# Optimization experiments

Hardware: AMD Instinct MI355X
Metric: run time of the kernel (lower is better)

The kernel has to match this reference:

```python
import jax, jax.numpy as jnp
import numpy as np

B, L, H, E = 8, 1024, 8, 64
HIST = 512


def setup_inputs() -> dict:
    key = jax.random.key(0)
    ks = jax.random.split(key, 6)
    shp = (B, L, H, E)
    q, k, v, qd, kd, vd = (jax.random.normal(kk, shp, dtype=jnp.float32) for kk in ks)
    # DoubleTriangularCausalMask surrogate: strictly-upper-triangular causal mask (diagonal=1)
    attn_mask = jnp.triu(jnp.ones((L, L), dtype=bool), k=1)[None, None]  # (1,1,L,S)
    return {
        "queries": q, "keys": k, "values": v,
        "queries_drawn": qd, "keys_drawn": kd, "values_drawn": vd,
        "attn_mask": attn_mask, "history_len": HIST,
    }


def reference(queries, keys, values, queries_drawn, keys_drawn, values_drawn, attn_mask, history_len):
    # drawn_y=True branch of FullFixedTimeCausalConstructiveAttention with history_len set.
    B, L, H, E = queries.shape
    scale = 1.0 / float(np.sqrt(E))
    hist = history_len
    idx = jnp.arange(hist, L)

    # queries[:, hist:] = queries_drawn[:, hist:]
    q_eff = jnp.concatenate([queries[:, :hist], queries_drawn[:, hist:]], axis=1)

    scores = jnp.einsum('blhe,bshe->bhls', q_eff, keys)  # (B,H,L,S)
    # diagonal positions l>=hist use drawn keys: q_eff[l] . keys_drawn[l]
    diag_scores = jnp.einsum('blhe,blhe->bhl', q_eff[:, hist:], keys_drawn[:, hist:])
    scores = scores.at[:, :, idx, idx].set(diag_scores)

    scores = jnp.where(attn_mask, -jnp.inf, scores)
    A = jax.nn.softmax(scale * scores, axis=-1)  # (B,H,L,S); dropout rate 0 in eval

    # values substitution on the diagonal (l==s, l>=hist) is a rank-1 correction;
    # avoids materializing the torch (B,H,D,L,S) repeated tensor.
    V = jnp.einsum('bhls,bshd->blhd', A, values)
    diag_A = A[:, :, idx, idx]                      # (B,H,L-hist)
    delta = values_drawn[:, hist:] - values[:, hist:]  # (B,L-hist,H,D)
    V = V.at[:, hist:].add(jnp.transpose(diag_A, (0, 2, 1))[..., None] * delta)
    return V
```

## Files before the change

kernel.cpp:

```cpp
#include <hip/hip_runtime.h>

#define LL   1024
#define HH   8
#define EE   64
#define KSTR 72

#define SCALE2 0.18033688011112043f

typedef _Float16 f16;
typedef _Float16 v8h  __attribute__((ext_vector_type(8)));
typedef _Float16 h2   __attribute__((ext_vector_type(2)));
typedef float    v4f  __attribute__((ext_vector_type(4)));
typedef int      v2i  __attribute__((ext_vector_type(2)));

union U8 { v8h v; h2 h[4]; };

__device__ __forceinline__ float fexp2(float x) {
#if __has_builtin(__builtin_amdgcn_exp2f)
  return __builtin_amdgcn_exp2f(x);
#else
  return __expf(x * 0.6931471805599453f);
#endif
}

__device__ __forceinline__ h2 pkh2(float a, float b) {
#if __has_builtin(__builtin_amdgcn_cvt_pkrtz)
  return __builtin_bit_cast(h2, __builtin_amdgcn_cvt_pkrtz(a, b));
#else
  h2 r; r[0] = (f16)a; r[1] = (f16)b; return r;
#endif
}

__device__ __forceinline__ float red4max(float x) {
#if __has_builtin(__builtin_amdgcn_permlane16_swap) && __has_builtin(__builtin_amdgcn_permlane32_swap)
  int xi = __float_as_int(x);
  v2i a = __builtin_amdgcn_permlane16_swap(xi, xi, false, false);
  float m = fmaxf(__int_as_float(a.x), __int_as_float(a.y));
  int mi = __float_as_int(m);
  v2i b = __builtin_amdgcn_permlane32_swap(mi, mi, false, false);
  return fmaxf(__int_as_float(b.x), __int_as_float(b.y));
#else
  x = fmaxf(x, __shfl_xor(x, 16));
  return fmaxf(x, __shfl_xor(x, 32));
#endif
}

__device__ __forceinline__ float red4sum(float x) {
#if __has_builtin(__builtin_amdgcn_permlane16_swap) && __has_builtin(__builtin_amdgcn_permlane32_swap)
  int xi = __float_as_int(x);
  v2i a = __builtin_amdgcn_permlane16_swap(xi, xi, false, false);
  float s = __int_as_float(a.x) + __int_as_float(a.y);
  int si = __float_as_int(s);
  v2i b = __builtin_amdgcn_permlane32_swap(si, si, false, false);
  return __int_as_float(b.x) + __int_as_float(b.y);
#else
  x += __shfl_xor(x, 16);
  return x + __shfl_xor(x, 32);
#endif
}

__device__ __forceinline__ void load16f(const float* __restrict__ p, float* __restrict__ f) {
  const float4* p4 = reinterpret_cast<const float4*>(p);
  float4 a = p4[0], b = p4[1], c = p4[2], d = p4[3];
  f[0]=a.x;  f[1]=a.y;  f[2]=a.z;  f[3]=a.w;
  f[4]=b.x;  f[5]=b.y;  f[6]=b.z;  f[7]=b.w;
  f[8]=c.x;  f[9]=c.y;  f[10]=c.z; f[11]=c.w;
  f[12]=d.x; f[13]=d.y; f[14]=d.z; f[15]=d.w;
}

__device__ __forceinline__ void load8f(const float* __restrict__ p, float* __restrict__ f) {
  const float4* p4 = reinterpret_cast<const float4*>(p);
  float4 a = p4[0], b = p4[1];
  f[0]=a.x; f[1]=a.y; f[2]=a.z; f[3]=a.w;
  f[4]=b.x; f[5]=b.y; f[6]=b.z; f[7]=b.w;
}

struct TileState {
  v4f   o[4];
  float m, l, pd;
};

__device__ __forceinline__ void softmax_pack(
    TileState& st, const v4f* __restrict__ S, bool dt, bool drawn, float zdq,
    int qlocal, const int* __restrict__ kb, int lq, U8& A0, U8& A1)
{
  float z[4][4];
#pragma unroll
  for (int nb = 0; nb < 4; ++nb)
#pragma unroll
    for (int r = 0; r < 4; ++r) z[nb][r] = S[nb][r] * SCALE2;

  if (dt) {
#pragma unroll
    for (int nb = 0; nb < 4; ++nb) {
#pragma unroll
      for (int r = 0; r < 4; ++r) {
        const int kl = kb[nb] + r;
        if (kl > qlocal)                 z[nb][r] = -1e30f;
        else if (drawn && kl == qlocal)  z[nb][r] = zdq;
      }
    }
  }

  float a0 = fmaxf(fmaxf(z[0][0], z[0][1]), fmaxf(z[0][2], z[0][3]));
  float a1 = fmaxf(fmaxf(z[1][0], z[1][1]), fmaxf(z[1][2], z[1][3]));
  float a2 = fmaxf(fmaxf(z[2][0], z[2][1]), fmaxf(z[2][2], z[2][3]));
  float a3 = fmaxf(fmaxf(z[3][0], z[3][1]), fmaxf(z[3][2], z[3][3]));
  const float mx = red4max(fmaxf(fmaxf(a0, a1), fmaxf(a2, a3)));

  const float mn = fmaxf(st.m, mx);
  const float al = fexp2(st.m - mn);
  st.m = mn;

  float p[4][4], rsum = 0.f, pdl = 0.f;
#pragma unroll
  for (int nb = 0; nb < 4; ++nb) {
#pragma unroll
    for (int r = 0; r < 4; ++r) {
      const float pv = fexp2(z[nb][r] - mn);
      p[nb][r] = pv;
      rsum += pv;
      if (dt && drawn && (kb[nb] + r) == qlocal) pdl = pv;
    }
  }
  rsum = red4sum(rsum);
  if (dt && drawn) st.pd = red4sum(pdl);
  st.l = st.l * al + rsum;
#pragma unroll
  for (int nb = 0; nb < 4; ++nb)
#pragma unroll
    for (int r = 0; r < 4; ++r) st.o[nb][r] *= al;

  h2 wq[4][2];
#pragma unroll
  for (int nb = 0; nb < 4; ++nb) {
    wq[nb][0] = pkh2(p[nb][0], p[nb][1]);
    wq[nb][1] = pkh2(p[nb][2], p[nb][3]);
  }
  const bool swp = (lq & 1);
  A0.h[0] = swp ? wq[1][0] : wq[0][0];
  A0.h[1] = swp ? wq[1][1] : wq[0][1];
  A0.h[2] = swp ? wq[0][0] : wq[1][0];
  A0.h[3] = swp ? wq[0][1] : wq[1][1];
  A1.h[0] = swp ? wq[3][0] : wq[2][0];
  A1.h[1] = swp ? wq[3][1] : wq[2][1];
  A1.h[2] = swp ? wq[2][0] : wq[3][0];
  A1.h[3] = swp ? wq[2][1] : wq[3][1];
}

extern "C" __global__ __launch_bounds__(256, 2)
void ftcca_pair2(const float* __restrict__ Q,  const float* __restrict__ K,
                 const float* __restrict__ V,  const float* __restrict__ Qd,
                 const float* __restrict__ Kd, const float* __restrict__ Vd,
                 float* __restrict__ out)
{
  __shared__ f16   Ks[64 * KSTR];
  __shared__ f16   Vt[64 * KSTR];
  __shared__ float zdiag[64];

  const int bh  = blockIdx.x & 63;
  const int a   = blockIdx.x >> 6;
  const int qtA = 15 - a;
  const int qtB = a;
  const int b   = bh >> 3, h = bh & 7;
  const int t   = threadIdx.x;
  const int w    = t >> 6;
  const int lane = t & 63;
  const int ln   = lane & 15;
  const int lq   = lane >> 4;
  const int rs   = t >> 2;
  const int es0  = (t & 3) * 16;
  const int vr0  = (t >> 3) * 2;
  const int vd0  = (t & 7) * 8;

  const size_t base = ((size_t)b * LL * HH + h) * EE;
  const int ROWF = HH * EE;

  const int q2 = ln >> 2;
  int rk[4], kb[4];
  rk[0] = ln + ((q2 + 1) >> 1) * 8;
  rk[1] = ln + 4 + (q2 >> 1) * 8;
  rk[2] = rk[0] + 32;
  rk[3] = rk[1] + 32;
  kb[0] = 4 * lq + ((lq + 1) >> 1) * 8;
  kb[1] = 4 * lq + 4 + (lq >> 1) * 8;
  kb[2] = kb[0] + 32;
  kb[3] = kb[1] + 32;

  {
    const int l = qtA * 64 + rs;
    const float* qrow = Qd + base + (size_t)l * ROWF + es0;
    const float* krow = Kd + base + (size_t)l * ROWF + es0;
    float par = 0.f;
#pragma unroll
    for (int i = 0; i < 16; ++i) par += qrow[i] * krow[i];
    par += __shfl_xor(par, 1);
    par += __shfl_xor(par, 2);
    if ((t & 3) == 0) zdiag[rs] = SCALE2 * par;
  }

  const int rowt_q = w * 16 + ln;
  v8h qfA[2], qfB[2];
  {
    const float* pa = Qd + base + (size_t)(qtA * 64 + rowt_q) * ROWF;
    const float* pb = Q  + base + (size_t)(qtB * 64 + rowt_q) * ROWF;
#pragma unroll
    for (int c = 0; c < 2; ++c) {
      const float* xa = pa + 32 * c + 8 * lq;
      const float* xb = pb + 32 * c + 8 * lq;
#pragma unroll
      for (int j = 0; j < 8; ++j) { qfA[c][j] = (f16)xa[j]; qfB[c][j] = (f16)xb[j]; }
    }
  }

  TileState stA, stB;
#pragma unroll
  for (int nb = 0; nb < 4; ++nb) { stA.o[nb] = (v4f){0,0,0,0}; stB.o[nb] = (v4f){0,0,0,0}; }
  stA.m = -1e30f; stA.l = 0.f; stA.pd = 0.f;
  stB.m = -1e30f; stB.l = 0.f; stB.pd = 0.f;

  const int qlocal = w * 16 + ln;

  float tk[16], tv[16];
  load16f(K + base + (size_t)rs * ROWF + es0, tk);
  load8f(V + base + (size_t)vr0 * ROWF + vd0, tv);
  load8f(V + base + (size_t)(vr0 + 1) * ROWF + vd0, tv + 8);

  for (int i = 0; i <= qtA; ++i) {
    __syncthreads();
    {
      v8h k0, k1;
#pragma unroll
      for (int j = 0; j < 8; ++j) { k0[j] = (f16)tk[j]; k1[j] = (f16)tk[8 + j]; }
      v8h* kd0 = reinterpret_cast<v8h*>(&Ks[rs * KSTR + es0]);
      kd0[0] = k0;
      kd0[1] = k1;
      const int vswz = vr0 >> 3;
#pragma unroll
      for (int dd = 0; dd < 8; ++dd) {
        const int d  = vd0 + dd;
        const int ch = (vswz ^ (d >> 3)) & 7;
        h2 val; val[0] = (f16)tv[dd]; val[1] = (f16)tv[8 + dd];
        *reinterpret_cast<h2*>(&Vt[d * KSTR + ch * 8 + (vr0 & 7)]) = val;
      }
    }
    __syncthreads();

    if (i < qtA) {
      const size_t r0 = (size_t)((i + 1) * 64);
      load16f(K + base + (r0 + rs) * ROWF + es0, tk);
      load8f(V + base + (r0 + vr0) * ROWF + vd0, tv);
      load8f(V + base + (r0 + vr0 + 1) * ROWF + vd0, tv + 8);
    }

    const bool doB = (i <= qtB);
    const bool dtA = (i == qtA);
    const bool dtB = (i == qtB);

    v8h k0f[4], k1f[4];
#pragma unroll
    for (int nb = 0; nb < 4; ++nb) {
      const f16* krow = &Ks[rk[nb] * KSTR + 8 * lq];
      k0f[nb] = *reinterpret_cast<const v8h*>(krow);
      k1f[nb] = *reinterpret_cast<const v8h*>(krow + 32);
    }

    v4f SA[4], SB[4];
#pragma unroll
    for (int nb = 0; nb < 4; ++nb) {
      v4f acc = (v4f){0.f, 0.f, 0.f, 0.f};
      acc = __builtin_amdgcn_mfma_f32_16x16x32_f16(k0f[nb], qfA[0], acc, 0, 0, 0);
      acc = __builtin_amdgcn_mfma_f32_16x16x32_f16(k1f[nb], qfA[1], acc, 0, 0, 0);
      SA[nb] = acc;
    }
    if (doB) {
#pragma unroll
      for (int nb = 0; nb < 4; ++nb) {
        v4f acc = (v4f){0.f, 0.f, 0.f, 0.f};
        acc = __builtin_amdgcn_mfma_f32_16x16x32_f16(k0f[nb], qfB[0], acc, 0, 0, 0);
        acc = __builtin_amdgcn_mfma_f32_16x16x32_f16(k1f[nb], qfB[1], acc, 0, 0, 0);
        SB[nb] = acc;
      }
    }

    U8 pA0, pA1, pB0, pB1;
    const float zdq = dtA ? zdiag[qlocal] : 0.f;
    softmax_pack(stA, SA, dtA, true,  zdq, qlocal, kb, lq, pA0, pA1);
    if (doB)
      softmax_pack(stB, SB, dtB, false, 0.f, qlocal, kb, lq, pB0, pB1);

#pragma unroll
    for (int nb = 0; nb < 4; ++nb) {
      const int d   = nb * 16 + ln;
      const int dsw = (d >> 3) & 7;
      const f16* vbase = &Vt[d * KSTR];
      v8h v0 = *reinterpret_cast<const v8h*>(vbase + (((lq    ) ^ dsw) & 7) * 8);
      v8h v1 = *reinterpret_cast<const v8h*>(vbase + (((lq + 4) ^ dsw) & 7) * 8);
      stA.o[nb] = __builtin_amdgcn_mfma_f32_16x16x32_f16(v0, pA0.v, stA.o[nb], 0, 0, 0);
      stA.o[nb] = __builtin_amdgcn_mfma_f32_16x16x32_f16(v1, pA1.v, stA.o[nb], 0, 0, 0);
      if (doB) {
        stB.o[nb] = __builtin_amdgcn_mfma_f32_16x16x32_f16(v0, pB0.v, stB.o[nb], 0, 0, 0);
        stB.o[nb] = __builtin_amdgcn_mfma_f32_16x16x32_f16(v1, pB1.v, stB.o[nb], 0, 0, 0);
      }
    }
  }

  {
    const float inv = 1.f / stA.l;
    const float pdinv = stA.pd * inv;
    const int lrow = qtA * 64 + w * 16 + ln;
#pragma unroll
    for (int nb = 0; nb < 4; ++nb) {
      const int d0 = nb * 16 + lq * 4;
      const size_t g = base + (size_t)lrow * ROWF + d0;
      float4 vd4 = *reinterpret_cast<const float4*>(Vd + g);
      float4 v4  = *reinterpret_cast<const float4*>(V + g);
      float4 o4;
      o4.x = stA.o[nb][0] * inv + pdinv * (vd4.x - v4.x);
      o4.y = stA.o[nb][1] * inv + pdinv * (vd4.y - v4.y);
      o4.z = stA.o[nb][2] * inv + pdinv * (vd4.z - v4.z);
      o4.w = stA.o[nb][3] * inv + pdinv * (vd4.w - v4.w);
      *reinterpret_cast<float4*>(out + g) = o4;
    }
  }
  {
    const float inv = 1.f / stB.l;
    const int lrow = qtB * 64 + w * 16 + ln;
#pragma unroll
    for (int nb = 0; nb < 4; ++nb) {
      const int d0 = nb * 16 + lq * 4;
      const size_t g = base + (size_t)lrow * ROWF + d0;
      float4 o4;
      o4.x = stB.o[nb][0] * inv;
      o4.y = stB.o[nb][1] * inv;
      o4.z = stB.o[nb][2] * inv;
      o4.w = stB.o[nb][3] * inv;
      *reinterpret_cast<float4*>(out + g) = o4;
    }
  }
}

extern "C" void kernel_launch(void* const* d_in, const int* in_sizes, int n_in,
                              void* d_out, int out_size, void* d_ws, size_t ws_size,
                              hipStream_t stream) {
  const float* q  = (const float*)d_in[0];
  const float* k  = (const float*)d_in[1];
  const float* v  = (const float*)d_in[2];
  const float* qd = (const float*)d_in[3];
  const float* kd = (const float*)d_in[4];
  const float* vd = (const float*)d_in[5];
  float* out = (float*)d_out;

  ftcca_pair2<<<dim3(512), dim3(256), 0, stream>>>(q, k, v, qd, kd, vd, out);
}
```

Measured before the change: 151.0 us.

## Process 128-key tiles per iteration instead of 64 in flash attention loop

Doubles the key/value tile per loop iteration to 128 rows, halving the number of barrier-synchronised iterations and softmax rescales. The V tile is transposed into a wider shared buffer with 4-row packed stores, and the softmax/pack routine handles eight score blocks. In exchange it raises register and LDS pressure, and diagonal tiles now compute a partly masked extra 64-key half.

```diff
diff --git a/kernel.cpp b/kernel.cpp
--- a/kernel.cpp
+++ b/kernel.cpp
@@ -4,12 +4,14 @@
 #define HH   8
 #define EE   64
 #define KSTR 72
+#define VSTR 136
 
 #define SCALE2 0.18033688011112043f
 
 typedef _Float16 f16;
 typedef _Float16 v8h  __attribute__((ext_vector_type(8)));
 typedef _Float16 h2   __attribute__((ext_vector_type(2)));
+typedef _Float16 h4   __attribute__((ext_vector_type(4)));
 typedef float    v4f  __attribute__((ext_vector_type(4)));
 typedef int      v2i  __attribute__((ext_vector_type(2)));
 
@@ -80,47 +82,52 @@
   float m, l, pd;
 };
 
-__device__ __forceinline__ void softmax_pack(
+__device__ __forceinline__ void softmax_pack8(
     TileState& st, const v4f* __restrict__ S, bool dt, bool drawn, float zdq,
-    int qlocal, const int* __restrict__ kb, int lq, U8& A0, U8& A1)
+    int qrel, const int* __restrict__ kbB, int lq, U8* __restrict__ P)
 {
-  float z[4][4];
-#pragma unroll
-  for (int nb = 0; nb < 4; ++nb)
+  float z[8][4];
+#pragma unroll
+  for (int nb = 0; nb < 8; ++nb)
 #pragma unroll
     for (int r = 0; r < 4; ++r) z[nb][r] = S[nb][r] * SCALE2;
 
   if (dt) {
 #pragma unroll
-    for (int nb = 0; nb < 4; ++nb) {
+    for (int nb = 0; nb < 8; ++nb) {
+      const int kl0 = kbB[nb & 1] + (nb >> 1) * 32;
 #pragma unroll
       for (int r = 0; r < 4; ++r) {
-        const int kl = kb[nb] + r;
-        if (kl > qlocal)                 z[nb][r] = -1e30f;
-        else if (drawn && kl == qlocal)  z[nb][r] = zdq;
-      }
-    }
-  }
-
-  float a0 = fmaxf(fmaxf(z[0][0], z[0][1]), fmaxf(z[0][2], z[0][3]));
-  float a1 = fmaxf(fmaxf(z[1][0], z[1][1]), fmaxf(z[1][2], z[1][3]));
-  float a2 = fmaxf(fmaxf(z[2][0], z[2][1]), fmaxf(z[2][2], z[2][3]));
-  float a3 = fmaxf(fmaxf(z[3][0], z[3][1]), fmaxf(z[3][2], z[3][3]));
-  const float mx = red4max(fmaxf(fmaxf(a0, a1), fmaxf(a2, a3)));
+        const int kl = kl0 + r;
+        if (kl > qrel)                 z[nb][r] = -1e30f;
+        else if (drawn && kl == qrel)  z[nb][r] = zdq;
+      }
+    }
+  }
+
+  float mloc = z[0][0];
+#pragma unroll
+  for (int nb = 0; nb < 8; ++nb) {
+    float a01 = fmaxf(z[nb][0], z[nb][1]);
+    float a23 = fmaxf(z[nb][2], z[nb][3]);
+    mloc = fmaxf(mloc, fmaxf(a01, a23));
+  }
+  const float mx = red4max(mloc);
 
   const float mn = fmaxf(st.m, mx);
   const float al = fexp2(st.m - mn);
   st.m = mn;
 
-  float p[4][4], rsum = 0.f, pdl = 0.f;
-#pragma unroll
-  for (int nb = 0; nb < 4; ++nb) {
+  float p[8][4], rsum = 0.f, pdl = 0.f;
+#pragma unroll
+  for (int nb = 0; nb < 8; ++nb) {
+    const int kl0 = kbB[nb & 1] + (nb >> 1) * 32;
 #pragma unroll
     for (int r = 0; r < 4; ++r) {
       const float pv = fexp2(z[nb][r] - mn);
       p[nb][r] = pv;
       rsum += pv;
-      if (dt && drawn && (kb[nb] + r) == qlocal) pdl = pv;
+      if (dt && drawn && (kl0 + r) == qrel) pdl = pv;
     }
   }
   rsum = red4sum(rsum);
@@ -131,31 +138,30 @@
 #pragma unroll
     for (int r = 0; r < 4; ++r) st.o[nb][r] *= al;
 
-  h2 wq[4][2];
-#pragma unroll
-  for (int nb = 0; nb < 4; ++nb) {
+  h2 wq[8][2];
+#pragma unroll
+  for (int nb = 0; nb < 8; ++nb) {
     wq[nb][0] = pkh2(p[nb][0], p[nb][1]);
     wq[nb][1] = pkh2(p[nb][2], p[nb][3]);
   }
   const bool swp = (lq & 1);
-  A0.h[0] = swp ? wq[1][0] : wq[0][0];
-  A0.h[1] = swp ? wq[1][1] : wq[0][1];
-  A0.h[2] = swp ? wq[0][0] : wq[1][0];
-  A0.h[3] = swp ? wq[0][1] : wq[1][1];
-  A1.h[0] = swp ? wq[3][0] : wq[2][0];
-  A1.h[1] = swp ? wq[3][1] : wq[2][1];
-  A1.h[2] = swp ? wq[2][0] : wq[3][0];
-  A1.h[3] = swp ? wq[2][1] : wq[3][1];
+#pragma unroll
+  for (int c = 0; c < 4; ++c) {
+    P[c].h[0] = swp ? wq[2 * c + 1][0] : wq[2 * c][0];
+    P[c].h[1] = swp ? wq[2 * c + 1][1] : wq[2 * c][1];
+    P[c].h[2] = swp ? wq[2 * c][0] : wq[2 * c + 1][0];
+    P[c].h[3] = swp ? wq[2 * c][1] : wq[2 * c + 1][1];
+  }
 }
 
 extern "C" __global__ __launch_bounds__(256, 2)
-void ftcca_pair2(const float* __restrict__ Q,  const float* __restrict__ K,
-                 const float* __restrict__ V,  const float* __restrict__ Qd,
-                 const float* __restrict__ Kd, const float* __restrict__ Vd,
-                 float* __restrict__ out)
+void ftcca_k128(const float* __restrict__ Q,  const float* __restrict__ K,
+                const float* __restrict__ V,  const float* __restrict__ Qd,
+                const float* __restrict__ Kd, const float* __restrict__ Vd,
+                float* __restrict__ out)
 {
-  __shared__ f16   Ks[64 * KSTR];
-  __shared__ f16   Vt[64 * KSTR];
+  __shared__ f16   Ks[128 * KSTR];
+  __shared__ f16   Vt[64 * VSTR];
   __shared__ float zdiag[64];
 
   const int bh  = blockIdx.x & 63;
@@ -170,22 +176,18 @@
   const int lq   = lane >> 4;
   const int rs   = t >> 2;
   const int es0  = (t & 3) * 16;
-  const int vr0  = (t >> 3) * 2;
+  const int vr0  = (t >> 3) * 4;
   const int vd0  = (t & 7) * 8;
 
   const size_t base = ((size_t)b * LL * HH + h) * EE;
   const int ROWF = HH * EE;
 
   const int q2 = ln >> 2;
-  int rk[4], kb[4];
-  rk[0] = ln + ((q2 + 1) >> 1) * 8;
-  rk[1] = ln + 4 + (q2 >> 1) * 8;
-  rk[2] = rk[0] + 32;
-  rk[3] = rk[1] + 32;
-  kb[0] = 4 * lq + ((lq + 1) >> 1) * 8;
-  kb[1] = 4 * lq + 4 + (lq >> 1) * 8;
-  kb[2] = kb[0] + 32;
-  kb[3] = kb[1] + 32;
+  int rkB[2], kbB[2];
+  rkB[0] = ln + ((q2 + 1) >> 1) * 8;
+  rkB[1] = ln + 4 + (q2 >> 1) * 8;
+  kbB[0] = 4 * lq + ((lq + 1) >> 1) * 8;
+  kbB[1] = 4 * lq + 4 + (lq >> 1) * 8;
 
   {
     const int l = qtA * 64 + rs;
@@ -220,87 +222,100 @@
   stB.m = -1e30f; stB.l = 0.f; stB.pd = 0.f;
 
   const int qlocal = w * 16 + ln;
-
-  float tk[16], tv[16];
+  const int itersA = (qtA >> 1) + 1;
+  const int dIA    = qtA >> 1;
+  const int dIB    = qtB >> 1;
+  const int qrelA  = ((qtA & 1) << 6) + qlocal;
+  const int qrelB  = ((qtB & 1) << 6) + qlocal;
+
+  float tk[32], tv[32];
   load16f(K + base + (size_t)rs * ROWF + es0, tk);
-  load8f(V + base + (size_t)vr0 * ROWF + vd0, tv);
-  load8f(V + base + (size_t)(vr0 + 1) * ROWF + vd0, tv + 8);
-
-  for (int i = 0; i <= qtA; ++i) {
+  load16f(K + base + (size_t)(rs + 64) * ROWF + es0, tk + 16);
+#pragma unroll
+  for (int j = 0; j < 4; ++j)
+    load8f(V + base + (size_t)(vr0 + j) * ROWF + vd0, tv + 8 * j);
+
+  for (int i = 0; i < itersA; ++i) {
     __syncthreads();
     {
-      v8h k0, k1;
-#pragma unroll
-      for (int j = 0; j < 8; ++j) { k0[j] = (f16)tk[j]; k1[j] = (f16)tk[8 + j]; }
-      v8h* kd0 = reinterpret_cast<v8h*>(&Ks[rs * KSTR + es0]);
-      kd0[0] = k0;
-      kd0[1] = k1;
+#pragma unroll
+      for (int half = 0; half < 2; ++half) {
+        v8h k0, k1;
+#pragma unroll
+        for (int j = 0; j < 8; ++j) { k0[j] = (f16)tk[16 * half + j]; k1[j] = (f16)tk[16 * half + 8 + j]; }
+        v8h* kd0 = reinterpret_cast<v8h*>(&Ks[(rs + 64 * half) * KSTR + es0]);
+        kd0[0] = k0;
+        kd0[1] = k1;
+      }
       const int vswz = vr0 >> 3;
 #pragma unroll
       for (int dd = 0; dd < 8; ++dd) {
         const int d  = vd0 + dd;
-        const int ch = (vswz ^ (d >> 3)) & 7;
-        h2 val; val[0] = (f16)tv[dd]; val[1] = (f16)tv[8 + dd];
-        *reinterpret_cast<h2*>(&Vt[d * KSTR + ch * 8 + (vr0 & 7)]) = val;
+        const int ch = vswz ^ (d >> 3);
+        h4 val;
+        val[0] = (f16)tv[dd];      val[1] = (f16)tv[8 + dd];
+        val[2] = (f16)tv[16 + dd]; val[3] = (f16)tv[24 + dd];
+        *reinterpret_cast<h4*>(&Vt[d * VSTR + ch * 8 + (vr0 & 7)]) = val;
       }
     }
     __syncthreads();
 
-    if (i < qtA) {
-      const size_t r0 = (size_t)((i + 1) * 64);
+    if (i < itersA - 1) {
+      const size_t r0 = (size_t)((i + 1) * 128);
       load16f(K + base + (r0 + rs) * ROWF + es0, tk);
-      load8f(V + base + (r0 + vr0) * ROWF + vd0, tv);
-      load8f(V + base + (r0 + vr0 + 1) * ROWF + vd0, tv + 8);
-    }
-
-    const bool doB = (i <= qtB);
-    const bool dtA = (i == qtA);
-    const bool dtB = (i == qtB);
-
-    v8h k0f[4], k1f[4];
+      load16f(K + base + (r0 + rs + 64) * ROWF + es0, tk + 16);
+#pragma unroll
+      for (int j = 0; j < 4; ++j)
+        load8f(V + base + (r0 + vr0 + j) * ROWF + vd0, tv + 8 * j);
+    }
+
+    const bool doB = (i <= dIB);
+    const bool dtA = (i == dIA);
+    const bool dtB = (i == dIB);
+
+    v4f SA[8], SB[8];
+#pragma unroll
+    for (int nb = 0; nb < 8; ++nb) {
+      const int row = rkB[nb & 1] + (nb >> 1) * 32;
+      const f16* krow = &Ks[row * KSTR + 8 * lq];
+      v8h k0 = *reinterpret_cast<const v8h*>(krow);
+      v8h k1 = *reinterpret_cast<const v8h*>(krow + 32);
+      v4f acc = (v4f){0.f, 0.f, 0.f, 0.f};
+      acc = __builtin_amdgcn_mfma_f32_16x16x32_f16(k0, qfA[0], acc, 0, 0, 0);
+      acc = __builtin_amdgcn_mfma_f32_16x16x32_f16(k1, qfA[1], acc, 0, 0, 0);
+      SA[nb] = acc;
+      if (doB) {
+        v4f accb = (v4f){0.f, 0.f, 0.f, 0.f};
+        accb = __builtin_amdgcn_mfma_f32_16x16x32_f16(k0, qfB[0], accb, 0, 0, 0);
+        accb = __builtin_amdgcn_mfma_f32_16x16x32_f16(k1, qfB[1], accb, 0, 0, 0);
+        SB[nb] = accb;
+      }
+    }
+
+    U8 PA[4], PB[4];
+    const float zdq = dtA ? zdiag[qlocal] : 0.f;
+    softmax_pack8(stA, SA, dtA, true,  zdq, qrelA, kbB, lq, PA);
+    if (doB)
+      softmax_pack8(stB, SB, dtB, false, 0.f, qrelB, kbB, lq, PB);
+
 #pragma unroll
     for (int nb = 0; nb < 4; ++nb) {
-      const f16* krow = &Ks[rk[nb] * KSTR + 8 * lq];
-      k0f[nb] = *reinterpret_cast<const v8h*>(krow);
-      k1f[nb] = *reinterpret_cast<const v8h*>(krow + 32);
-    }
-
-    v4f SA[4], SB[4];
-#pragma unroll
-    for (int nb = 0; nb < 4; ++nb) {
-      v4f acc = (v4f){0.f, 0.f, 0.f, 0.f};
-      acc = __builtin_amdgcn_mfma_f32_16x16x32_f16(k0f[nb], qfA[0], acc, 0, 0, 0);
-      acc = __builtin_amdgcn_mfma_f32_16x16x32_f16(k1f[nb], qfA[1], acc, 0, 0, 0);
-      SA[nb] = acc;
-    }
-    if (doB) {
-#pragma unroll
-      for (int nb = 0; nb < 4; ++nb) {
-        v4f acc = (v4f){0.f, 0.f, 0.f, 0.f};
-        acc = __builtin_amdgcn_mfma_f32_16x16x32_f16(k0f[nb], qfB[0], acc, 0, 0, 0);
-        acc = __builtin_amdgcn_mfma_f32_16x16x32_f16(k1f[nb], qfB[1], acc, 0, 0, 0);
-        SB[nb] = acc;
-      }
-    }
-
-    U8 pA0, pA1, pB0, pB1;
-    const float zdq = dtA ? zdiag[qlocal] : 0.f;
-    softmax_pack(stA, SA, dtA, true,  zdq, qlocal, kb, lq, pA0, pA1);
-    if (doB)
-      softmax_pack(stB, SB, dtB, false, 0.f, qlocal, kb, lq, pB0, pB1);
-
-#pragma unroll
-    for (int nb = 0; nb < 4; ++nb) {
-      const int d   = nb * 16 + ln;
-      const int dsw = (d >> 3) & 7;
-      const f16* vbase = &Vt[d * KSTR];
-      v8h v0 = *reinterpret_cast<const v8h*>(vbase + (((lq    ) ^ dsw) & 7) * 8);
-      v8h v1 = *reinterpret_cast<const v8h*>(vbase + (((lq + 4) ^ dsw) & 7) * 8);
-      stA.o[nb] = __builtin_amdgcn_mfma_f32_16x16x32_f16(v0, pA0.v, stA.o[nb], 0, 0, 0);
-      stA.o[nb] = __builtin_amdgcn_mfma_f32_16x16x32_f16(v1, pA1.v, stA.o[nb], 0, 0, 0);
+      const int d    = nb * 16 + ln;
+      const int dxor = d >> 3;
+      const f16* vbase = &Vt[d * VSTR];
+      v8h vf[4];
+#pragma unroll
+      for (int c = 0; c < 4; ++c) {
+        const int ch = (4 * c + lq) ^ dxor;
+        vf[c] = *reinterpret_cast<const v8h*>(vbase + ch * 8);
+      }
+#pragma unroll
+      for (int c = 0; c < 4; ++c)
+        stA.o[nb] = __builtin_amdgcn_mfma_f32_16x16x32_f16(vf[c], PA[c].v, stA.o[nb], 0, 0, 0);
       if (doB) {
-        stB.o[nb] = __builtin_amdgcn_mfma_f32_16x16x32_f16(v0, pB0.v, stB.o[nb], 0, 0, 0);
-        stB.o[nb] = __builtin_amdgcn_mfma_f32_16x16x32_f16(v1, pB1.v, stB.o[nb], 0, 0, 0);
+#pragma unroll
+        for (int c = 0; c < 4; ++c)
+          stB.o[nb] = __builtin_amdgcn_mfma_f32_16x16x32_f16(vf[c], PB[c].v, stB.o[nb], 0, 0, 0);
       }
     }
   }
@@ -351,5 +366,5 @@
   const float* vd = (const float*)d_in[5];
   float* out = (float*)d_out;
 
-  ftcca_pair2<<<dim3(512), dim3(256), 0, stream>>>(q, k, v, qd, kd, vd, out);
-}
+  ftcca_k128<<<dim3(512), dim3(256), 0, stream>>>(q, k, v, qd, kd, vd, out);
+}
```

Result: slower. 159.7 us (+5.7%).
